# Kernel tuning notes

Measured on AMD Instinct MI355X. Metric: run time of the kernel, lower is better.

## Reference

```python
import jax, jax.numpy as jnp
import numpy as np

N_NODES = 50000
N_EDGES = 1600000
N_REL = 8
D_IN = 128
D_HID = 128
D_OUT = 64
N_POOL = 256


def setup_inputs() -> dict:
    key = jax.random.key(0)
    ks = jax.random.split(key, 10)
    x = jax.random.uniform(ks[0], (N_NODES, D_IN), dtype=jnp.float32)
    edge_index = jax.random.randint(ks[1], (2, N_EDGES), 0, N_NODES)
    edge_type = jax.random.randint(ks[2], (N_EDGES,), 0, N_REL)
    pool_indices = jax.random.randint(ks[3], (N_POOL,), 0, N_NODES)
    s1 = 1.0 / np.sqrt(D_IN)
    s2 = 1.0 / np.sqrt(D_HID)
    W1 = jax.random.normal(ks[4], (N_REL, D_IN, D_HID), dtype=jnp.float32) * s1
    root1 = jax.random.normal(ks[5], (D_IN, D_HID), dtype=jnp.float32) * s1
    b1 = jnp.zeros((D_HID,), jnp.float32)
    W2 = jax.random.normal(ks[6], (N_REL, D_HID, D_OUT), dtype=jnp.float32) * s2
    root2 = jax.random.normal(ks[7], (D_HID, D_OUT), dtype=jnp.float32) * s2
    b2 = jnp.zeros((D_OUT,), jnp.float32)
    return {"x": x, "edge_index": edge_index, "edge_type": edge_type,
            "pool_indices": pool_indices, "W1": W1, "root1": root1, "b1": b1,
            "W2": W2, "root2": root2, "b2": b2}


def rgcn_layer(h, edge_index, edge_type, W, root, b):
    # PyG RGCNConv: out = h @ root + sum_r mean_{j in N_r(i)} (h_j @ W_r) + b
    src, dst = edge_index[0], edge_index[1]
    n = h.shape[0]
    r = W.shape[0]
    hW = jnp.einsum('nd,rdh->rnh', h, W)          # (R, N, H)
    msg = hW[edge_type, src]                      # (E, H) gather per edge
    seg = edge_type * n + dst                     # per-(relation, dst) segment
    agg = jax.ops.segment_sum(msg, seg, num_segments=r * n)
    agg = agg.reshape(r, n, -1)
    cnt = jax.ops.segment_sum(jnp.ones(msg.shape[0], h.dtype), seg,
                              num_segments=r * n).reshape(r, n, 1)
    mean = agg / jnp.maximum(cnt, 1.0)            # per-relation mean
    return mean.sum(0) + h @ root + b


def reference(x, edge_index, edge_type, pool_indices, W1, root1, b1, W2, root2, b2):
    h = jax.nn.relu(rgcn_layer(x, edge_index, edge_type, W1, root1, b1))
    node_embeddings = rgcn_layer(h, edge_index, edge_type, W2, root2, b2)
    selected_embeddings = node_embeddings[pool_indices]       # (P, D_OUT)
    type_features = x[pool_indices, :3]                       # (P, 3)
    weights = jnp.array([4.0, 1.0, 2.0], dtype=x.dtype)
    entity_weights = type_features @ weights                  # (P,)
    sum_of_weights = jnp.sum(entity_weights) + 1e-9
    pooled = jnp.sum(selected_embeddings * entity_weights[:, None], axis=0,
                     keepdims=True) / sum_of_weights          # (1, D_OUT)
    return pooled
```

## Files before the change

kernel.cpp:

```cpp
#include <hip/hip_runtime.h>

#define N_NODES 50000
#define N_EDGES 1600000
#define N_REL   8
#define D_IN    128
#define D_HID   128
#define D_OUT   64
#define N_POOL  256

#define CAP_S   12288
#define BUCKET  32
#define NSEG_N  (N_REL * N_NODES)

typedef short v8s __attribute__((ext_vector_type(8)));
typedef float v4f __attribute__((ext_vector_type(4)));

constexpr size_t OFF_FILLC  = 0;
constexpr size_t ZERO_ELEMS = NSEG_N;
constexpr size_t OFF_PBIT   = ZERO_ELEMS;
constexpr size_t OFF_SBIT   = OFF_PBIT + 2048;
constexpr size_t OFF_CTR    = OFF_SBIT + 2048;
constexpr size_t OFF_SNODES = OFF_CTR + 16;
constexpr size_t OFF_SID    = OFF_SNODES + CAP_S;
constexpr size_t OFF_SRCSLOT= OFF_SID + N_NODES;
constexpr size_t OFF_AGG1B  = OFF_SRCSLOT + (size_t)NSEG_N * BUCKET;
constexpr size_t OFF_XALL   = OFF_AGG1B + (size_t)CAP_S * 8 * 64;
constexpr size_t OFF_WT     = OFF_XALL + (size_t)N_NODES * 64;
constexpr size_t OFF_H      = OFF_WT + (size_t)1152 * 128 / 2;
constexpr size_t OFF_EMB    = OFF_H + (size_t)CAP_S * D_HID;
constexpr size_t TOTAL_ELEMS= OFF_EMB + (size_t)N_POOL * D_OUT;

__device__ __forceinline__ unsigned short f2bf(float f) {
  union { float f; unsigned u; } v; v.f = f;
  unsigned r = v.u + 0x7FFFu + ((v.u >> 16) & 1u);
  return (unsigned short)(r >> 16);
}
__device__ __forceinline__ float bfLo(unsigned v) { return __uint_as_float(v << 16); }
__device__ __forceinline__ float bfHi(unsigned v) { return __uint_as_float(v & 0xFFFF0000u); }

__global__ __launch_bounds__(256) void k_init(
    const int* __restrict__ pool, const float* __restrict__ x,
    const float* __restrict__ W1, const float* __restrict__ root1,
    float* __restrict__ ws) {
  unsigned* pBit = (unsigned*)(ws + OFF_PBIT);
  unsigned* sBit = (unsigned*)(ws + OFF_SBIT);
  int*      ctr  = (int*)(ws + OFF_CTR);
  unsigned long long* xall8 = (unsigned long long*)(ws + OFF_XALL);
  unsigned short* Wt = (unsigned short*)(ws + OFF_WT);
  float4*   emb4 = (float4*)(ws + OFF_EMB);
  int tid = threadIdx.x, bid = blockIdx.x;
  int gtid = bid * 256 + tid, gthr = gridDim.x * 256;
  int wave = tid >> 6, lane = tid & 63;

  float4 z = {0.f, 0.f, 0.f, 0.f};
  for (int i = gtid; i < (int)(ZERO_ELEMS / 4); i += gthr) ((float4*)ws)[i] = z;
  for (int i = gtid; i < N_POOL * D_OUT / 4; i += gthr) emb4[i] = z;

  if (bid == 0) {
    for (int i = tid; i < 2048; i += 256) { pBit[i] = 0u; sBit[i] = 0u; }
    if (tid < 16) ctr[tid] = 0;
    __syncthreads();
    int node = pool[tid];
    unsigned bit = 1u << (node & 31);
    atomicOr(&pBit[node >> 5], bit);
    atomicOr(&sBit[node >> 5], bit);
  }

  int gw = (bid - 1) * 4 + wave;
  if (bid >= 1 && gw < 288) {
    int kt = gw >> 3, nt = gw & 7;
    int k0 = kt * 32 + ((lane >> 4) << 3);
    int n = nt * 16 + (lane & 15);
    v8s frag;
#pragma unroll
    for (int j = 0; j < 8; j++) {
      int kg = k0 + j;
      float v = (kg < 1024) ? W1[(size_t)kg * D_HID + n]
                            : root1[(size_t)(kg - 1024) * D_HID + n];
      frag[j] = (short)f2bf(v);
    }
    ((v8s*)Wt)[gw * 64 + lane] = frag;
  }

  for (int i = gtid; i < N_NODES * 32; i += gthr) {
    float4 v = ((const float4*)x)[i];
    unsigned lo = ((unsigned)f2bf(v.y) << 16) | f2bf(v.x);
    unsigned hi = ((unsigned)f2bf(v.w) << 16) | f2bf(v.z);
    xall8[i] = (unsigned long long)lo | ((unsigned long long)hi << 32);
  }
}

__global__ __launch_bounds__(256) void k_pass1(
    const int* __restrict__ EI, const int* __restrict__ pool,
    unsigned* __restrict__ sBit) {
  __shared__ unsigned pb[2048];
  int tid = threadIdx.x;
  for (int i = tid; i < 2048; i += 256) pb[i] = 0u;
  __syncthreads();
  { int node = pool[tid]; atomicOr(&pb[node >> 5], 1u << (node & 31)); }
  __syncthreads();
  int idx = blockIdx.x * 256 + tid;
  if (idx >= N_EDGES / 4) return;
  int4 d4 = ((const int4*)(EI + N_EDGES))[idx];
  int d[4] = {d4.x, d4.y, d4.z, d4.w};
#pragma unroll
  for (int i = 0; i < 4; i++) {
    int dst = d[i];
    if ((pb[dst >> 5] >> (dst & 31)) & 1u) {
      int src = EI[idx * 4 + i];
      atomicOr(&sBit[src >> 5], 1u << (src & 31));
    }
  }
}

__global__ __launch_bounds__(256) void k_fillc(
    const int* __restrict__ EI, const int* __restrict__ ET,
    const unsigned* __restrict__ sBit,
    int* __restrict__ fillCtr, int* __restrict__ srcSlot,
    int* __restrict__ sNodes, int* __restrict__ sId, int* __restrict__ ctr) {
  __shared__ int ismem[8];
  int tid = threadIdx.x, bid = blockIdx.x;
  int wave = tid >> 6, lane = tid & 63;

  if (bid < 196) {
    int node = bid * 256 + tid;
    bool sp = (node < N_NODES) && ((sBit[node >> 5] >> (node & 31)) & 1u);
    unsigned long long m = __ballot(sp);
    if (lane == 0) ismem[wave] = __popcll(m);
    __syncthreads();
    if (tid == 0) {
      int tot = ismem[0] + ismem[1] + ismem[2] + ismem[3];
      ismem[4] = tot ? atomicAdd(&ctr[1], tot) : 0;
    }
    __syncthreads();
    if (sp) {
      int off = ismem[4];
      for (int w2 = 0; w2 < wave; w2++) off += ismem[w2];
      int id = off + __popcll(m & ((1ull << lane) - 1ull));
      if (id < CAP_S) { sNodes[id] = node; sId[node] = id; }
    }
  }

  int idx = bid * 256 + tid;
  if (idx >= N_EDGES / 4) return;
  int4 d4 = ((const int4*)(EI + N_EDGES))[idx];
  int d[4] = {d4.x, d4.y, d4.z, d4.w};
  bool any = false;
#pragma unroll
  for (int i = 0; i < 4; i++)
    any |= ((sBit[d[i] >> 5] >> (d[i] & 31)) & 1u) != 0u;
  if (!any) return;
  int4 t4 = ((const int4*)ET)[idx];
  int4 s4 = ((const int4*)EI)[idx];
  int t[4] = {t4.x, t4.y, t4.z, t4.w};
  int s[4] = {s4.x, s4.y, s4.z, s4.w};
#pragma unroll
  for (int i = 0; i < 4; i++) {
    int dst = d[i];
    if ((sBit[dst >> 5] >> (dst & 31)) & 1u) {
      int seg = (dst << 3) + t[i];
      int slot = atomicAdd(&fillCtr[seg], 1);
      if (slot < BUCKET) srcSlot[(size_t)seg * BUCKET + slot] = s[i];
    }
  }
}

__global__ __launch_bounds__(256) void k_gather(
    const int* __restrict__ fillCtr, const int* __restrict__ srcSlot,
    const unsigned long long* __restrict__ xall8, const int* __restrict__ ctr,
    const int* __restrict__ sNodes, unsigned long long* __restrict__ agg1b8) {
  int sCount = ctr[1]; if (sCount > CAP_S) sCount = CAP_S;
  int total = sCount << 3;
  int lane = threadIdx.x & 63;
  int half = lane >> 5, hl = lane & 31;
  int wstride = gridDim.x << 2;
  for (int p = (blockIdx.x << 2) + (threadIdx.x >> 6); 2 * p < total; p += wstride) {
    int w = 2 * p + half;
    if (w < total) {
      int node = sNodes[w >> 3];
      int seg = (node << 3) + (w & 7);
      int cnt = fillCtr[seg];
      if (cnt > BUCKET) cnt = BUCKET;
      const int* slot = srcSlot + (size_t)seg * BUCKET;
      float a0 = 0.f, a1 = 0.f, a2 = 0.f, a3 = 0.f;
      int i = 0;
      for (; i + 4 <= cnt; i += 4) {
        int s0 = slot[i + 0];
        int s1 = slot[i + 1];
        int s2 = slot[i + 2];
        int s3 = slot[i + 3];
        unsigned long long v0 = xall8[(size_t)s0 * 32 + hl];
        unsigned long long v1 = xall8[(size_t)s1 * 32 + hl];
        unsigned long long v2 = xall8[(size_t)s2 * 32 + hl];
        unsigned long long v3 = xall8[(size_t)s3 * 32 + hl];
        unsigned l0 = (unsigned)v0, h0 = (unsigned)(v0 >> 32);
        unsigned l1 = (unsigned)v1, h1 = (unsigned)(v1 >> 32);
        unsigned l2 = (unsigned)v2, h2 = (unsigned)(v2 >> 32);
        unsigned l3 = (unsigned)v3, h3 = (unsigned)(v3 >> 32);
        a0 += (bfLo(l0) + bfLo(l1)) + (bfLo(l2) + bfLo(l3));
        a1 += (bfHi(l0) + bfHi(l1)) + (bfHi(l2) + bfHi(l3));
        a2 += (bfLo(h0) + bfLo(h1)) + (bfLo(h2) + bfLo(h3));
        a3 += (bfHi(h0) + bfHi(h1)) + (bfHi(h2) + bfHi(h3));
      }
      for (; i < cnt; i++) {
        unsigned long long v = xall8[(size_t)slot[i] * 32 + hl];
        unsigned lo = (unsigned)v, hi = (unsigned)(v >> 32);
        a0 += bfLo(lo); a1 += bfHi(lo);
        a2 += bfLo(hi); a3 += bfHi(hi);
      }
      float inv = 1.0f / fmaxf((float)cnt, 1.0f);
      unsigned w0 = ((unsigned)f2bf(a1 * inv) << 16) | f2bf(a0 * inv);
      unsigned w1 = ((unsigned)f2bf(a3 * inv) << 16) | f2bf(a2 * inv);
      agg1b8[(size_t)w * 32 + hl] =
          (unsigned long long)w0 | ((unsigned long long)w1 << 32);
    }
  }
}

__global__ __launch_bounds__(256) void k_gemm1(
    const unsigned* __restrict__ agg1b, const unsigned* __restrict__ xall,
    const unsigned short* __restrict__ Wt, const float* __restrict__ b1,
    const int* __restrict__ sNodes, const int* __restrict__ ctr,
    float* __restrict__ h) {
  int sCount = ctr[1]; if (sCount > CAP_S) sCount = CAP_S;
  int s0 = blockIdx.x * 16;
  if (s0 >= sCount) return;
  int wave = threadIdx.x >> 6, lane = threadIdx.x & 63;
  int quad = lane >> 4, mn = lane & 15;
  int srow = s0 + mn;
  int g = (srow < sCount) ? sNodes[srow] : 0;
  v4f acc0 = (v4f){0.f, 0.f, 0.f, 0.f};
  v4f acc1 = (v4f){0.f, 0.f, 0.f, 0.f};
  const v8s* WtF = (const v8s*)Wt;
  for (int kt = 0; kt < 36; kt++) {
    const unsigned short* aptr;
    if (kt < 32) {
      int r = kt >> 2;
      int d0 = (kt & 3) * 32 + quad * 8;
      aptr = (const unsigned short*)agg1b + ((size_t)((srow << 3) + r) * 128 + d0);
    } else {
      int d0 = (kt - 32) * 32 + quad * 8;
      aptr = (const unsigned short*)xall + ((size_t)g * 128 + d0);
    }
    v8s afrag = *(const v8s*)aptr;
    const v8s* wrow = WtF + (size_t)(kt * 8 + wave * 2) * 64 + lane;
    acc0 = __builtin_amdgcn_mfma_f32_16x16x32_bf16(afrag, wrow[0],  acc0, 0, 0, 0);
    acc1 = __builtin_amdgcn_mfma_f32_16x16x32_bf16(afrag, wrow[64], acc1, 0, 0, 0);
  }
  int col0 = wave * 32 + mn;
  int col1 = col0 + 16;
  float bv0 = b1[col0], bv1 = b1[col1];
#pragma unroll
  for (int reg = 0; reg < 4; reg++) {
    int s = s0 + quad * 4 + reg;
    if (s < sCount) {
      h[(size_t)s * D_HID + col0] = fmaxf(acc0[reg] + bv0, 0.0f);
      h[(size_t)s * D_HID + col1] = fmaxf(acc1[reg] + bv1, 0.0f);
    }
  }
}

__global__ __launch_bounds__(256) void k_gemmB(
    const float* __restrict__ x, const int* __restrict__ pool,
    const float* __restrict__ W2, const float* __restrict__ root2,
    const float* __restrict__ b2, const int* __restrict__ fillCtr,
    const int* __restrict__ srcSlot, const int* __restrict__ sId,
    int* __restrict__ ctr, const float* __restrict__ h,
    float* __restrict__ emb, float* __restrict__ out) {
  __shared__ float smem[896];
  __shared__ int lastFlag;
  int tid = threadIdx.x, wave = tid >> 6, lane = tid & 63;
  int pl = blockIdx.x >> 1, half = blockIdx.x & 1;
  {
    int nodeP = pool[pl];
    float* a = smem;
    float* partial = smem + 640;
    int r = half * 4 + wave;
    int seg = (nodeP << 3) + r;
    int cnt = fillCtr[seg]; if (cnt > BUCKET) cnt = BUCKET;
    const int* sl = srcSlot + (size_t)seg * BUCKET;
    float s0 = 0.f, s1 = 0.f;
    for (int i = 0; i < cnt; i++) {
      int row = sId[sl[i]];
      float2 v = ((const float2*)h)[(size_t)row * 64 + lane];
      s0 += v.x; s1 += v.y;
    }
    float inv = 1.0f / fmaxf((float)cnt, 1.0f);
    a[wave * 128 + lane * 2]     = s0 * inv;
    a[wave * 128 + lane * 2 + 1] = s1 * inv;
    if (half == 1 && tid < 128) {
      int rowP = sId[nodeP];
      a[512 + tid] = h[(size_t)rowP * D_HID + tid];
    }
    __syncthreads();
    float acc = 0.0f;
    int kbase = half * 512 + wave * 128;
#pragma unroll 8
    for (int j = 0; j < 128; j++)
      acc += a[wave * 128 + j] * W2[(size_t)(kbase + j) * D_OUT + lane];
    if (half == 1) {
      int rbase = wave * 32;
#pragma unroll 4
      for (int j = 0; j < 32; j++)
        acc += a[512 + rbase + j] * root2[(size_t)(rbase + j) * D_OUT + lane];
    }
    partial[tid] = acc;
    __syncthreads();
    if (tid < 64) {
      float r4 = partial[tid] + partial[tid + 64] + partial[tid + 128] + partial[tid + 192];
      if (half == 0) r4 += b2[tid];
      unsafeAtomicAdd(&emb[(size_t)pl * D_OUT + tid], r4);
    }
  }
  __syncthreads();
  if (tid == 0) {
    __builtin_amdgcn_fence(__ATOMIC_RELEASE, "agent");
    int old = __hip_atomic_fetch_add(&ctr[2], 1, __ATOMIC_RELAXED,
                                     __HIP_MEMORY_SCOPE_AGENT);
    lastFlag = (old == (int)gridDim.x - 1) ? 1 : 0;
  }
  __syncthreads();
  if (lastFlag == 0) return;
  if (tid == 0) __builtin_amdgcn_fence(__ATOMIC_ACQUIRE, "agent");
  __syncthreads();
  {
    float* ew  = smem;
    float* part= smem + 512;
    int node = pool[tid];
    const float* xr = x + (size_t)node * D_IN;
    ew[tid] = 4.0f * xr[0] + 1.0f * xr[1] + 2.0f * xr[2];
    __syncthreads();
    float acc = 0.0f;
    int j0 = wave * 64;
#pragma unroll 8
    for (int j = j0; j < j0 + 64; j++)
      acc += ew[j] * emb[(size_t)j * D_OUT + lane];
    part[wave * 64 + lane] = acc;
    __syncthreads();
    if (tid < 64) {
      float sw = 0.0f;
      for (int j = 0; j < N_POOL; j++) sw += ew[j];
      float r4 = part[tid] + part[64 + tid] + part[128 + tid] + part[192 + tid];
      out[tid] = r4 / (sw + 1e-9f);
    }
  }
}

extern "C" void kernel_launch(void* const* d_in, const int* in_sizes, int n_in,
                              void* d_out, int out_size, void* d_ws, size_t ws_size,
                              hipStream_t stream) {
  const float* x     = (const float*)d_in[0];
  const int*   EI    = (const int*)  d_in[1];
  const int*   ET    = (const int*)  d_in[2];
  const int*   pool  = (const int*)  d_in[3];
  const float* W1    = (const float*)d_in[4];
  const float* root1 = (const float*)d_in[5];
  const float* b1    = (const float*)d_in[6];
  const float* W2    = (const float*)d_in[7];
  const float* root2 = (const float*)d_in[8];
  const float* b2    = (const float*)d_in[9];
  float* out = (float*)d_out;
  float* ws  = (float*)d_ws;

  int*      fillCtr = (int*)(ws + OFF_FILLC);
  unsigned* sBit    = (unsigned*)(ws + OFF_SBIT);
  int*      ctr     = (int*)(ws + OFF_CTR);
  int*      sNodes  = (int*)(ws + OFF_SNODES);
  int*      sId     = (int*)(ws + OFF_SID);
  int*      srcSlot = (int*)(ws + OFF_SRCSLOT);
  unsigned* agg1b   = (unsigned*)(ws + OFF_AGG1B);
  unsigned* xall    = (unsigned*)(ws + OFF_XALL);
  unsigned short* Wt = (unsigned short*)(ws + OFF_WT);
  float*    h       = ws + OFF_H;
  float*    emb     = ws + OFF_EMB;

  k_init<<<1024, 256, 0, stream>>>(pool, x, W1, root1, ws);
  k_pass1<<<(N_EDGES / 4 + 255) / 256, 256, 0, stream>>>(EI, pool, sBit);
  k_fillc<<<(N_EDGES / 4 + 255) / 256, 256, 0, stream>>>(
      EI, ET, sBit, fillCtr, srcSlot, sNodes, sId, ctr);
  k_gather<<<4096, 256, 0, stream>>>(
      fillCtr, srcSlot, (const unsigned long long*)xall, ctr, sNodes,
      (unsigned long long*)agg1b);
  k_gemm1<<<CAP_S / 16, 256, 0, stream>>>(agg1b, xall, Wt, b1, sNodes, ctr, h);
  k_gemmB<<<2 * N_POOL, 256, 0, stream>>>(
      x, pool, W2, root2, b2, fillCtr, srcSlot, sId, ctr, h, emb, out);
}
```

Measured before the change: 176.0 us.

## Use nontemporal streaming loads, dual-segment gather, and 32-row GEMM tiles

Streaming reads of x and edge arrays, and the bf16 x store, now use nontemporal load/store builtins so they do not pollute the cache. The gather kernel has each half-wave process two segments at once, interleaving their loads to raise memory-level parallelism. The first GEMM now computes 32 rows per block, so each B fragment is reused across two A tiles, which halves weight fragment loads per output. The dual-segment loop pays for this with predication waste when the two counts differ, and it uses more registers.

```diff
diff --git a/kernel.cpp b/kernel.cpp
--- a/kernel.cpp
+++ b/kernel.cpp
@@ -14,6 +14,8 @@
 
 typedef short v8s __attribute__((ext_vector_type(8)));
 typedef float v4f __attribute__((ext_vector_type(4)));
+typedef int   v4i __attribute__((ext_vector_type(4)));
+typedef float v4ff __attribute__((ext_vector_type(4)));
 
 constexpr size_t OFF_FILLC  = 0;
 constexpr size_t ZERO_ELEMS = NSEG_N;
@@ -83,10 +85,11 @@
   }
 
   for (int i = gtid; i < N_NODES * 32; i += gthr) {
-    float4 v = ((const float4*)x)[i];
-    unsigned lo = ((unsigned)f2bf(v.y) << 16) | f2bf(v.x);
-    unsigned hi = ((unsigned)f2bf(v.w) << 16) | f2bf(v.z);
-    xall8[i] = (unsigned long long)lo | ((unsigned long long)hi << 32);
+    v4ff v = __builtin_nontemporal_load((const v4ff*)x + i);
+    unsigned lo = ((unsigned)f2bf(v[1]) << 16) | f2bf(v[0]);
+    unsigned hi = ((unsigned)f2bf(v[3]) << 16) | f2bf(v[2]);
+    unsigned long long w8 = (unsigned long long)lo | ((unsigned long long)hi << 32);
+    __builtin_nontemporal_store(w8, &xall8[i]);
   }
 }
 
@@ -101,11 +104,10 @@
   __syncthreads();
   int idx = blockIdx.x * 256 + tid;
   if (idx >= N_EDGES / 4) return;
-  int4 d4 = ((const int4*)(EI + N_EDGES))[idx];
-  int d[4] = {d4.x, d4.y, d4.z, d4.w};
+  v4i d4 = __builtin_nontemporal_load((const v4i*)(EI + N_EDGES) + idx);
 #pragma unroll
   for (int i = 0; i < 4; i++) {
-    int dst = d[i];
+    int dst = d4[i];
     if ((pb[dst >> 5] >> (dst & 31)) & 1u) {
       int src = EI[idx * 4 + i];
       atomicOr(&sBit[src >> 5], 1u << (src & 31));
@@ -143,24 +145,21 @@
 
   int idx = bid * 256 + tid;
   if (idx >= N_EDGES / 4) return;
-  int4 d4 = ((const int4*)(EI + N_EDGES))[idx];
-  int d[4] = {d4.x, d4.y, d4.z, d4.w};
+  v4i d4 = __builtin_nontemporal_load((const v4i*)(EI + N_EDGES) + idx);
   bool any = false;
 #pragma unroll
   for (int i = 0; i < 4; i++)
-    any |= ((sBit[d[i] >> 5] >> (d[i] & 31)) & 1u) != 0u;
+    any |= ((sBit[d4[i] >> 5] >> (d4[i] & 31)) & 1u) != 0u;
   if (!any) return;
-  int4 t4 = ((const int4*)ET)[idx];
-  int4 s4 = ((const int4*)EI)[idx];
-  int t[4] = {t4.x, t4.y, t4.z, t4.w};
-  int s[4] = {s4.x, s4.y, s4.z, s4.w};
+  v4i t4 = __builtin_nontemporal_load((const v4i*)ET + idx);
+  v4i s4 = __builtin_nontemporal_load((const v4i*)EI + idx);
 #pragma unroll
   for (int i = 0; i < 4; i++) {
-    int dst = d[i];
+    int dst = d4[i];
     if ((sBit[dst >> 5] >> (dst & 31)) & 1u) {
-      int seg = (dst << 3) + t[i];
+      int seg = (dst << 3) + t4[i];
       int slot = atomicAdd(&fillCtr[seg], 1);
-      if (slot < BUCKET) srcSlot[(size_t)seg * BUCKET + slot] = s[i];
+      if (slot < BUCKET) srcSlot[(size_t)seg * BUCKET + slot] = s4[i];
     }
   }
 }
@@ -173,45 +172,61 @@
   int total = sCount << 3;
   int lane = threadIdx.x & 63;
   int half = lane >> 5, hl = lane & 31;
-  int wstride = gridDim.x << 2;
-  for (int p = (blockIdx.x << 2) + (threadIdx.x >> 6); 2 * p < total; p += wstride) {
-    int w = 2 * p + half;
-    if (w < total) {
-      int node = sNodes[w >> 3];
-      int seg = (node << 3) + (w & 7);
-      int cnt = fillCtr[seg];
-      if (cnt > BUCKET) cnt = BUCKET;
-      const int* slot = srcSlot + (size_t)seg * BUCKET;
-      float a0 = 0.f, a1 = 0.f, a2 = 0.f, a3 = 0.f;
-      int i = 0;
-      for (; i + 4 <= cnt; i += 4) {
-        int s0 = slot[i + 0];
-        int s1 = slot[i + 1];
-        int s2 = slot[i + 2];
-        int s3 = slot[i + 3];
-        unsigned long long v0 = xall8[(size_t)s0 * 32 + hl];
-        unsigned long long v1 = xall8[(size_t)s1 * 32 + hl];
-        unsigned long long v2 = xall8[(size_t)s2 * 32 + hl];
-        unsigned long long v3 = xall8[(size_t)s3 * 32 + hl];
-        unsigned l0 = (unsigned)v0, h0 = (unsigned)(v0 >> 32);
-        unsigned l1 = (unsigned)v1, h1 = (unsigned)(v1 >> 32);
-        unsigned l2 = (unsigned)v2, h2 = (unsigned)(v2 >> 32);
-        unsigned l3 = (unsigned)v3, h3 = (unsigned)(v3 >> 32);
-        a0 += (bfLo(l0) + bfLo(l1)) + (bfLo(l2) + bfLo(l3));
-        a1 += (bfHi(l0) + bfHi(l1)) + (bfHi(l2) + bfHi(l3));
-        a2 += (bfLo(h0) + bfLo(h1)) + (bfLo(h2) + bfLo(h3));
-        a3 += (bfHi(h0) + bfHi(h1)) + (bfHi(h2) + bfHi(h3));
+  int nHW = gridDim.x << 3;
+  int hwid = (((blockIdx.x << 2) + (threadIdx.x >> 6)) << 1) + half;
+  for (int base = 0; base < total; base += (nHW << 1)) {
+    int wA = base + hwid;
+    if (wA >= total) break;
+    int wB = wA + nHW;
+    bool doB = wB < total;
+    int nodeA = sNodes[wA >> 3];
+    int segA = (nodeA << 3) + (wA & 7);
+    int cA = fillCtr[segA]; if (cA > BUCKET) cA = BUCKET;
+    int segB = 0, cB = 0;
+    if (doB) {
+      int nodeB = sNodes[wB >> 3];
+      segB = (nodeB << 3) + (wB & 7);
+      cB = fillCtr[segB]; if (cB > BUCKET) cB = BUCKET;
+    }
+    const int* sA = srcSlot + (size_t)segA * BUCKET;
+    const int* sB = srcSlot + (size_t)segB * BUCKET;
+    float a0A = 0.f, a1A = 0.f, a2A = 0.f, a3A = 0.f;
+    float a0B = 0.f, a1B = 0.f, a2B = 0.f, a3B = 0.f;
+    int mx = cA > cB ? cA : cB;
+    for (int i = 0; i < mx; i += 4) {
+#pragma unroll
+      for (int k2 = 0; k2 < 4; k2++) {
+        int ii = i + k2;
+        if (ii < cA) {
+          unsigned long long v = xall8[(size_t)sA[ii] * 32 + hl];
+          unsigned lo = (unsigned)v, hi = (unsigned)(v >> 32);
+          a0A += bfLo(lo); a1A += bfHi(lo);
+          a2A += bfLo(hi); a3A += bfHi(hi);
+        }
       }
-      for (; i < cnt; i++) {
-        unsigned long long v = xall8[(size_t)slot[i] * 32 + hl];
-        unsigned lo = (unsigned)v, hi = (unsigned)(v >> 32);
-        a0 += bfLo(lo); a1 += bfHi(lo);
-        a2 += bfLo(hi); a3 += bfHi(hi);
+#pragma unroll
+      for (int k2 = 0; k2 < 4; k2++) {
+        int ii = i + k2;
+        if (ii < cB) {
+          unsigned long long v = xall8[(size_t)sB[ii] * 32 + hl];
+          unsigned lo = (unsigned)v, hi = (unsigned)(v >> 32);
+          a0B += bfLo(lo); a1B += bfHi(lo);
+          a2B += bfLo(hi); a3B += bfHi(hi);
+        }
       }
-      float inv = 1.0f / fmaxf((float)cnt, 1.0f);
-      unsigned w0 = ((unsigned)f2bf(a1 * inv) << 16) | f2bf(a0 * inv);
-      unsigned w1 = ((unsigned)f2bf(a3 * inv) << 16) | f2bf(a2 * inv);
-      agg1b8[(size_t)w * 32 + hl] =
+    }
+    {
+      float inv = 1.0f / fmaxf((float)cA, 1.0f);
+      unsigned w0 = ((unsigned)f2bf(a1A * inv) << 16) | f2bf(a0A * inv);
+      unsigned w1 = ((unsigned)f2bf(a3A * inv) << 16) | f2bf(a2A * inv);
+      agg1b8[(size_t)wA * 32 + hl] =
+          (unsigned long long)w0 | ((unsigned long long)w1 << 32);
+    }
+    if (doB) {
+      float inv = 1.0f / fmaxf((float)cB, 1.0f);
+      unsigned w0 = ((unsigned)f2bf(a1B * inv) << 16) | f2bf(a0B * inv);
+      unsigned w1 = ((unsigned)f2bf(a3B * inv) << 16) | f2bf(a2B * inv);
+      agg1b8[(size_t)wB * 32 + hl] =
           (unsigned long long)w0 | ((unsigned long long)w1 << 32);
     }
   }
@@ -223,39 +238,51 @@
     const int* __restrict__ sNodes, const int* __restrict__ ctr,
     float* __restrict__ h) {
   int sCount = ctr[1]; if (sCount > CAP_S) sCount = CAP_S;
-  int s0 = blockIdx.x * 16;
+  int s0 = blockIdx.x * 32;
   if (s0 >= sCount) return;
   int wave = threadIdx.x >> 6, lane = threadIdx.x & 63;
   int quad = lane >> 4, mn = lane & 15;
-  int srow = s0 + mn;
-  int g = (srow < sCount) ? sNodes[srow] : 0;
-  v4f acc0 = (v4f){0.f, 0.f, 0.f, 0.f};
-  v4f acc1 = (v4f){0.f, 0.f, 0.f, 0.f};
+  int srow0 = s0 + mn, srow1 = s0 + 16 + mn;
+  int g0 = (srow0 < sCount) ? sNodes[srow0] : 0;
+  int g1 = (srow1 < sCount) ? sNodes[srow1] : 0;
+  v4f acc00 = (v4f){0.f,0.f,0.f,0.f}, acc01 = (v4f){0.f,0.f,0.f,0.f};
+  v4f acc10 = (v4f){0.f,0.f,0.f,0.f}, acc11 = (v4f){0.f,0.f,0.f,0.f};
   const v8s* WtF = (const v8s*)Wt;
   for (int kt = 0; kt < 36; kt++) {
-    const unsigned short* aptr;
+    const unsigned short *ap0, *ap1;
     if (kt < 32) {
       int r = kt >> 2;
       int d0 = (kt & 3) * 32 + quad * 8;
-      aptr = (const unsigned short*)agg1b + ((size_t)((srow << 3) + r) * 128 + d0);
+      ap0 = (const unsigned short*)agg1b + ((size_t)((srow0 << 3) + r) * 128 + d0);
+      ap1 = (const unsigned short*)agg1b + ((size_t)((srow1 << 3) + r) * 128 + d0);
     } else {
       int d0 = (kt - 32) * 32 + quad * 8;
-      aptr = (const unsigned short*)xall + ((size_t)g * 128 + d0);
-    }
-    v8s afrag = *(const v8s*)aptr;
+      ap0 = (const unsigned short*)xall + ((size_t)g0 * 128 + d0);
+      ap1 = (const unsigned short*)xall + ((size_t)g1 * 128 + d0);
+    }
+    v8s af0 = *(const v8s*)ap0;
+    v8s af1 = *(const v8s*)ap1;
     const v8s* wrow = WtF + (size_t)(kt * 8 + wave * 2) * 64 + lane;
-    acc0 = __builtin_amdgcn_mfma_f32_16x16x32_bf16(afrag, wrow[0],  acc0, 0, 0, 0);
-    acc1 = __builtin_amdgcn_mfma_f32_16x16x32_bf16(afrag, wrow[64], acc1, 0, 0, 0);
+    v8s bf0 = wrow[0], bf1 = wrow[64];
+    acc00 = __builtin_amdgcn_mfma_f32_16x16x32_bf16(af0, bf0, acc00, 0, 0, 0);
+    acc01 = __builtin_amdgcn_mfma_f32_16x16x32_bf16(af0, bf1, acc01, 0, 0, 0);
+    acc10 = __builtin_amdgcn_mfma_f32_16x16x32_bf16(af1, bf0, acc10, 0, 0, 0);
+    acc11 = __builtin_amdgcn_mfma_f32_16x16x32_bf16(af1, bf1, acc11, 0, 0, 0);
   }
   int col0 = wave * 32 + mn;
   int col1 = col0 + 16;
   float bv0 = b1[col0], bv1 = b1[col1];
 #pragma unroll
   for (int reg = 0; reg < 4; reg++) {
-    int s = s0 + quad * 4 + reg;
-    if (s < sCount) {
-      h[(size_t)s * D_HID + col0] = fmaxf(acc0[reg] + bv0, 0.0f);
-      h[(size_t)s * D_HID + col1] = fmaxf(acc1[reg] + bv1, 0.0f);
+    int sA = s0 + quad * 4 + reg;
+    int sB = sA + 16;
+    if (sA < sCount) {
+      h[(size_t)sA * D_HID + col0] = fmaxf(acc00[reg] + bv0, 0.0f);
+      h[(size_t)sA * D_HID + col1] = fmaxf(acc01[reg] + bv1, 0.0f);
+    }
+    if (sB < sCount) {
+      h[(size_t)sB * D_HID + col0] = fmaxf(acc10[reg] + bv0, 0.0f);
+      h[(size_t)sB * D_HID + col1] = fmaxf(acc11[reg] + bv1, 0.0f);
     }
   }
 }
@@ -381,7 +408,7 @@
   k_gather<<<4096, 256, 0, stream>>>(
       fillCtr, srcSlot, (const unsigned long long*)xall, ctr, sNodes,
       (unsigned long long*)agg1b);
-  k_gemm1<<<CAP_S / 16, 256, 0, stream>>>(agg1b, xall, Wt, b1, sNodes, ctr, h);
+  k_gemm1<<<CAP_S / 32, 256, 0, stream>>>(agg1b, xall, Wt, b1, sNodes, ctr, h);
   k_gemmB<<<2 * N_POOL, 256, 0, stream>>>(
       x, pool, W2, root2, b2, fillCtr, srcSlot, sId, ctr, h, emb, out);
 }
```

Result: slower. 187.8 us (+6.7%).
